# Performance work log

Measured on AMD Instinct MI355X. Metric: run time of the kernel, lower is better.

Reference implementation:

```python
import jax, jax.numpy as jnp
import numpy as np

EMBED_DIM = 1024
NUM_HEADS = 16
HEAD_DIM = EMBED_DIM // NUM_HEADS
MAX_SEQ_LEN = 2048
B, T = 2, 2048


def setup_inputs() -> dict:
    key = jax.random.key(0)
    ks = jax.random.split(key, 12)
    d = EMBED_DIM
    s = lambda fan_in: 1.0 / np.sqrt(fan_in)
    return {
        "x": jax.random.normal(ks[0], (B, T, d), dtype=jnp.float32),
        "ln1_g": jnp.ones((d,), jnp.float32),
        "ln1_b": jnp.zeros((d,), jnp.float32),
        "w_attn": jax.random.normal(ks[1], (d, 3 * d), jnp.float32) * s(d),
        "b_attn": jnp.zeros((3 * d,), jnp.float32),
        "w_proj": jax.random.normal(ks[2], (d, d), jnp.float32) * s(d),
        "b_proj": jnp.zeros((d,), jnp.float32),
        "ln2_g": jnp.ones((d,), jnp.float32),
        "ln2_b": jnp.zeros((d,), jnp.float32),
        "w_fc": jax.random.normal(ks[3], (d, 4 * d), jnp.float32) * s(d),
        "b_fc": jnp.zeros((4 * d,), jnp.float32),
        "w_fc2": jax.random.normal(ks[4], (4 * d, d), jnp.float32) * s(4 * d),
        "b_fc2": jnp.zeros((d,), jnp.float32),
    }


def _layernorm(x, g, b, eps=1e-5):
    mu = jnp.mean(x, axis=-1, keepdims=True)
    var = jnp.var(x, axis=-1, keepdims=True)
    return (x - mu) * jax.lax.rsqrt(var + eps) * g + b


def _attention(x, w_attn, b_attn, w_proj, b_proj):
    b, t, c = x.shape
    qkv = x @ w_attn + b_attn  # [B,T,3C]
    q, k, v = jnp.split(qkv, 3, axis=-1)
    # [B,T,C] -> [B,H,T,Dh]
    rs = lambda a: a.reshape(b, t, NUM_HEADS, HEAD_DIM).transpose(0, 2, 1, 3)
    q, k, v = rs(q), rs(k), rs(v)
    wei = jnp.einsum("bhqd,bhkd->bhqk", q, k) * (HEAD_DIM ** -0.5)
    causal = jnp.tril(jnp.ones((t, t), bool))
    wei = jnp.where(causal, wei, -jnp.inf)
    wei = jax.nn.softmax(wei, axis=-1)  # attn_dropout is identity in eval mode
    out = jnp.einsum("bhqk,bhkd->bhqd", wei, v)
    out = out.transpose(0, 2, 1, 3).reshape(b, t, c)
    return out @ w_proj + b_proj  # resid_dropout identity in eval mode


def _ffn(x, w_fc, b_fc, w_fc2, b_fc2):
    h = jax.nn.gelu(x @ w_fc + b_fc, approximate=False)
    return h @ w_fc2 + b_fc2  # dropout identity in eval mode


def reference(x, ln1_g, ln1_b, w_attn, b_attn, w_proj, b_proj,
              ln2_g, ln2_b, w_fc, b_fc, w_fc2, b_fc2):
    x = x + _attention(_layernorm(x, ln1_g, ln1_b), w_attn, b_attn, w_proj, b_proj)
    x = x + _ffn(_layernorm(x, ln2_g, ln2_b), w_fc, b_fc, w_fc2, b_fc2)
    return x
```

## Files before the change

kernel.cpp:

```cpp
#include <hip/hip_runtime.h>

#define EMBED 1024
#define THREE_EMBED 3072
#define HEADS 16
#define HDIM 64
#define SEQ 2048
#define BATCH 2
#define MTOT 4096

typedef short bf16x8 __attribute__((ext_vector_type(8)));
typedef float f32x4 __attribute__((ext_vector_type(4)));

#define MFMA16(a, b, c) __builtin_amdgcn_mfma_f32_16x16x32_bf16(a, b, c, 0, 0, 0)

__device__ __forceinline__ unsigned short f2bf(float f) {
  union { float f; unsigned int u; } v; v.f = f;
  unsigned int r = v.u + 0x7fffu + ((v.u >> 16) & 1u);
  return (unsigned short)(r >> 16);
}

__device__ __forceinline__ float bf2f(unsigned short u) {
  union { unsigned int u; float f; } v;
  v.u = (unsigned int)u << 16;
  return v.f;
}

__device__ __forceinline__ void gload_lds16(const unsigned short* g, unsigned short* l) {
  __builtin_amdgcn_global_load_lds(
      (const __attribute__((address_space(1))) void*)g,
      (__attribute__((address_space(3))) void*)l, 16, 0, 0);
}

__device__ __forceinline__ void wait_vm0_barrier() {
  asm volatile("s_waitcnt vmcnt(0)" ::: "memory");
  __builtin_amdgcn_s_barrier();
}

template <int N>
__device__ __forceinline__ void wait_vmcnt() {
  if constexpr (N == 0) asm volatile("s_waitcnt vmcnt(0)" ::: "memory");
  else if constexpr (N == 1) asm volatile("s_waitcnt vmcnt(1)" ::: "memory");
  else if constexpr (N == 2) asm volatile("s_waitcnt vmcnt(2)" ::: "memory");
  else if constexpr (N == 3) asm volatile("s_waitcnt vmcnt(3)" ::: "memory");
  else if constexpr (N == 4) asm volatile("s_waitcnt vmcnt(4)" ::: "memory");
  else if constexpr (N == 6) asm volatile("s_waitcnt vmcnt(6)" ::: "memory");
  else if constexpr (N == 8) asm volatile("s_waitcnt vmcnt(8)" ::: "memory");
}

__device__ __forceinline__ void lds_fence() {
  asm volatile("s_waitcnt lgkmcnt(0)" ::: "memory");
  __builtin_amdgcn_sched_barrier(0);
}

__global__ __launch_bounds__(256) void k_transpose_all(
    const float* __restrict__ w_attn, const float* __restrict__ w_proj,
    const float* __restrict__ w_fc, const float* __restrict__ w_fc2,
    unsigned short* __restrict__ o_attn, unsigned short* __restrict__ o_proj,
    unsigned short* __restrict__ o_fc, unsigned short* __restrict__ o_fc2) {
  __shared__ float t[32][33];
  int bid = blockIdx.x;
  const float* in;
  unsigned short* out;
  int K, N, lid;
  if (bid < 3072) {
    in = w_attn; out = o_attn; K = 1024; N = 3072; lid = bid;
  } else if (bid < 4096) {
    in = w_proj; out = o_proj; K = 1024; N = 1024; lid = bid - 3072;
  } else if (bid < 8192) {
    in = w_fc; out = o_fc; K = 1024; N = 4096; lid = bid - 4096;
  } else {
    in = w_fc2; out = o_fc2; K = 4096; N = 1024; lid = bid - 8192;
  }
  int gx = N >> 5;
  int n0 = (lid % gx) * 32, k0 = (lid / gx) * 32;
  int tx = threadIdx.x & 31, ty = threadIdx.x >> 5;
#pragma unroll
  for (int i = 0; i < 32; i += 8)
    t[ty + i][tx] = in[(size_t)(k0 + ty + i) * N + n0 + tx];
  __syncthreads();
#pragma unroll
  for (int i = 0; i < 32; i += 8)
    out[(size_t)(n0 + ty + i) * K + k0 + tx] = f2bf(t[tx][ty + i]);
}

__global__ __launch_bounds__(256) void k_transpose_v(
    const unsigned short* __restrict__ qkv, unsigned short* __restrict__ Vt) {
  __shared__ unsigned short t[32][33];
  int tx = threadIdx.x & 31, ty = threadIdx.x >> 5;
  int t0 = blockIdx.x * 32;
  int d0 = (blockIdx.y & 1) * 32;
  int bh = blockIdx.y >> 1;
  int b = bh >> 4, h = bh & 15;
  const unsigned short* src = qkv + (size_t)b * SEQ * THREE_EMBED + 2 * EMBED + h * HDIM;
#pragma unroll
  for (int i = 0; i < 32; i += 8)
    t[ty + i][tx] = src[(size_t)(t0 + ty + i) * THREE_EMBED + d0 + tx];
  __syncthreads();
  unsigned short* dst = Vt + (size_t)bh * HDIM * SEQ;
#pragma unroll
  for (int i = 0; i < 32; i += 8)
    dst[(size_t)(d0 + ty + i) * SEQ + t0 + tx] = t[tx][ty + i];
}

__global__ __launch_bounds__(256) void k_layernorm(
    const float* __restrict__ x, const float* __restrict__ g,
    const float* __restrict__ b, unsigned short* __restrict__ out) {
  int row = blockIdx.x;
  int tid = threadIdx.x;
  const float4 xv = *(const float4*)(x + (size_t)row * EMBED + tid * 4);
  float s = xv.x + xv.y + xv.z + xv.w;
  float sq = xv.x * xv.x + xv.y * xv.y + xv.z * xv.z + xv.w * xv.w;
#pragma unroll
  for (int off = 1; off < 64; off <<= 1) {
    s += __shfl_xor(s, off);
    sq += __shfl_xor(sq, off);
  }
  __shared__ float red[8];
  int w = tid >> 6;
  if ((tid & 63) == 0) { red[w] = s; red[4 + w] = sq; }
  __syncthreads();
  s = red[0] + red[1] + red[2] + red[3];
  sq = red[4] + red[5] + red[6] + red[7];
  float mu = s * (1.0f / EMBED);
  float var = sq * (1.0f / EMBED) - mu * mu;
  float rs = rsqrtf(var + 1e-5f);
  float xs[4] = {xv.x, xv.y, xv.z, xv.w};
  unsigned short o[4];
#pragma unroll
  for (int c = 0; c < 4; c++) {
    int col = tid * 4 + c;
    o[c] = f2bf((xs[c] - mu) * rs * g[col] + b[col]);
  }
  *(ushort4*)(out + (size_t)row * EMBED + tid * 4) = *(const ushort4*)o;
}

template <int EPI>
__global__ __launch_bounds__(512, 2) void k_gemm8(
    const unsigned short* __restrict__ A, const unsigned short* __restrict__ Bt,
    const float* __restrict__ bias, const float* __restrict__ resid,
    float* __restrict__ outf, unsigned short* __restrict__ outb,
    int M, int N, int K) {
  __shared__ unsigned short lA[2][16384];
  __shared__ unsigned short lB[2][16384];
  int tid = threadIdx.x;
  int nwg = gridDim.x * gridDim.y;
  int bid = blockIdx.y * gridDim.x + blockIdx.x;
  int swz = (bid & 7) * (nwg >> 3) + (bid >> 3);
  int m0 = (swz / gridDim.x) * 256, n0 = (swz % gridDim.x) * 256;
  int lane = tid & 63, w = tid >> 6;
  int lr = lane & 15, lg = lane >> 4;
  int warow = (w >> 2) * 64;
  int wbrow = (w & 3) * 32;
  int rx = lr & 7;
  int colk[2] = {(lg ^ rx) * 8, ((4 + lg) ^ rx) * 8};
  f32x4 acc[8][4] = {};
  int swzk = ((lane & 7) ^ ((lane >> 3) & 7)) * 8;
  const unsigned short* gA[2];
  const unsigned short* gB[2];
#pragma unroll
  for (int i = 0; i < 2; i++) {
    int chrow = (w * 2 + i) * 8 + (lane >> 3);
    gA[i] = A + (size_t)(m0 + chrow) * K + swzk;
    gB[i] = Bt + (size_t)(n0 + chrow) * K + swzk;
  }
  int NT = K >> 6;
  auto stageA = [&](int h, int kt, int buf) {
    size_t goff = (size_t)(h * 128) * K + (size_t)kt * 64;
    int lo = h * 8192 + w * 1024;
    gload_lds16(gA[0] + goff, &lA[buf][lo]);
    gload_lds16(gA[1] + goff, &lA[buf][lo + 512]);
  };
  auto stageB = [&](int h, int kt, int buf) {
    size_t goff = (size_t)(h * 128) * K + (size_t)kt * 64;
    int lo = h * 8192 + w * 1024;
    gload_lds16(gB[0] + goff, &lB[buf][lo]);
    gload_lds16(gB[1] + goff, &lB[buf][lo + 512]);
  };
  bf16x8 aX[4][2], aY[4][2], b0[2][2], b1[2][2];
  auto rdA = [&](int buf, int mh, bf16x8 (&dst)[4][2]) {
#pragma unroll
    for (int ii = 0; ii < 4; ii++) {
      int ra = mh * 128 + warow + ii * 16 + lr;
#pragma unroll
      for (int ks = 0; ks < 2; ks++)
        dst[ii][ks] = *(const bf16x8*)&lA[buf][ra * 64 + colk[ks]];
    }
  };
  auto rdB = [&](int buf, int nh, bf16x8 (&dst)[2][2]) {
#pragma unroll
    for (int jj = 0; jj < 2; jj++) {
      int rb = nh * 128 + wbrow + jj * 16 + lr;
#pragma unroll
      for (int ks = 0; ks < 2; ks++)
        dst[jj][ks] = *(const bf16x8*)&lB[buf][rb * 64 + colk[ks]];
    }
  };
  auto mf = [&](int mh, int nh, bf16x8 (&aa)[4][2], bf16x8 (&bb)[2][2]) {
    __builtin_amdgcn_s_setprio(1);
#pragma unroll
    for (int ii = 0; ii < 4; ii++)
#pragma unroll
      for (int jj = 0; jj < 2; jj++)
#pragma unroll
        for (int ks = 0; ks < 2; ks++)
          acc[mh * 4 + ii][nh * 2 + jj] =
              MFMA16(aa[ii][ks], bb[jj][ks], acc[mh * 4 + ii][nh * 2 + jj]);
    __builtin_amdgcn_s_setprio(0);
  };
  stageA(0, 0, 0); stageB(0, 0, 0);
  stageB(1, 0, 0); stageA(1, 0, 0);
  wait_vmcnt<4>();
  __builtin_amdgcn_s_barrier();
  rdA(0, 0, aX);
  for (int t = 0; t < NT - 1; t++) {
    int cur = t & 1, nxt = cur ^ 1;
    rdB(cur, 0, b0);
    stageA(0, t + 1, nxt); stageB(0, t + 1, nxt);
    wait_vmcnt<4>();
    __builtin_amdgcn_s_barrier();
    lds_fence();
    mf(0, 0, aX, b0);
    rdB(cur, 1, b1);
    rdA(cur, 1, aY);
    __builtin_amdgcn_s_barrier();
    lds_fence();
    mf(0, 1, aX, b1);
    stageB(1, t + 1, nxt); stageA(1, t + 1, nxt);
    wait_vmcnt<4>();
    __builtin_amdgcn_s_barrier();
    lds_fence();
    mf(1, 1, aY, b1);
    rdA(nxt, 0, aX);
    __builtin_amdgcn_s_barrier();
    lds_fence();
    mf(1, 0, aY, b0);
  }
  {
    int cur = (NT - 1) & 1;
    rdB(cur, 0, b0);
    wait_vmcnt<0>();
    __builtin_amdgcn_s_barrier();
    lds_fence();
    mf(0, 0, aX, b0);
    rdB(cur, 1, b1);
    rdA(cur, 1, aY);
    lds_fence();
    mf(0, 1, aX, b1);
    mf(1, 1, aY, b1);
    mf(1, 0, aY, b0);
  }
#pragma unroll
  for (int i = 0; i < 8; i++) {
#pragma unroll
    for (int j = 0; j < 4; j++) {
      int col = n0 + (j >> 1) * 128 + wbrow + (j & 1) * 16 + lr;
      float bv = bias[col];
#pragma unroll
      for (int r = 0; r < 4; r++) {
        int row = m0 + (i >> 2) * 128 + warow + (i & 3) * 16 + lg * 4 + r;
        float v = acc[i][j][r] + bv;
        size_t idx = (size_t)row * N + col;
        if constexpr (EPI == 0) {
          outb[idx] = f2bf(v);
        } else if constexpr (EPI == 1) {
          outf[idx] = v + resid[idx];
        } else {
          float gv = 0.5f * v * (1.0f + erff(v * 0.70710678118654752f));
          outb[idx] = f2bf(gv);
        }
      }
    }
  }
}

template <int EPI>
__global__ __launch_bounds__(256) void k_gemmN(
    const unsigned short* __restrict__ A, const unsigned short* __restrict__ Bt,
    const float* __restrict__ bias, const float* __restrict__ resid,
    float* __restrict__ outf, unsigned short* __restrict__ outb,
    int M, int N, int K) {
  __shared__ unsigned short lA[3][128 * 64];
  __shared__ unsigned short lB[3][64 * 64];
  int tid = threadIdx.x;
  int nwg = gridDim.x * gridDim.y;
  int bid = blockIdx.y * gridDim.x + blockIdx.x;
  int swz = (bid & 7) * (nwg >> 3) + (bid >> 3);
  int m0 = (swz / gridDim.x) * 128, n0 = (swz % gridDim.x) * 64;
  int lane = tid & 63, w = tid >> 6;
  int wm = w * 32;
  int lr = lane & 15, lg = lane >> 4;
  int rx = lr & 7;
  int colk[2] = {(lg ^ rx) * 8, ((4 + lg) ^ rx) * 8};
  f32x4 acc[2][4] = {};
  int swzk = ((lane & 7) ^ ((lane >> 3) & 7)) * 8;
  const unsigned short* gsrc[6];
  int loff[6];
  bool isa[6];
#pragma unroll
  for (int c0 = 0; c0 < 6; c0++) {
    int c = w * 6 + c0;
    if (c < 16) {
      int row = c * 8 + (lane >> 3);
      gsrc[c0] = A + (size_t)(m0 + row) * K + swzk;
      loff[c0] = c * 512;
      isa[c0] = true;
    } else {
      int row = (c - 16) * 8 + (lane >> 3);
      gsrc[c0] = Bt + (size_t)(n0 + row) * K + swzk;
      loff[c0] = (c - 16) * 512;
      isa[c0] = false;
    }
  }
  auto stage = [&](int k0, int buf) {
#pragma unroll
    for (int c0 = 0; c0 < 6; c0++)
      gload_lds16(gsrc[c0] + k0, isa[c0] ? &lA[buf][loff[c0]] : &lB[buf][loff[c0]]);
  };
  auto compute = [&](int buf) {
    bf16x8 af[2][2], bf[4][2];
#pragma unroll
    for (int i = 0; i < 2; i++)
#pragma unroll
      for (int ks = 0; ks < 2; ks++)
        af[i][ks] = *(const bf16x8*)&lA[buf][(wm + i * 16 + lr) * 64 + colk[ks]];
#pragma unroll
    for (int j = 0; j < 4; j++)
#pragma unroll
      for (int ks = 0; ks < 2; ks++)
        bf[j][ks] = *(const bf16x8*)&lB[buf][(j * 16 + lr) * 64 + colk[ks]];
    __builtin_amdgcn_s_setprio(1);
#pragma unroll
    for (int i = 0; i < 2; i++)
#pragma unroll
      for (int j = 0; j < 4; j++)
#pragma unroll
        for (int ks = 0; ks < 2; ks++)
          acc[i][j] = MFMA16(af[i][ks], bf[j][ks], acc[i][j]);
    __builtin_amdgcn_s_setprio(0);
  };
  int nt = K >> 6;
  stage(0, 0);
  stage(64, 1);
  wait_vmcnt<6>();
  __builtin_amdgcn_s_barrier();
  int c0 = 0, c1 = 1, c2 = 2;
  for (int t = 0; t < nt - 2; t++) {
    stage((t + 2) * 64, c2);
    compute(c0);
    wait_vmcnt<6>();
    __builtin_amdgcn_s_barrier();
    int tmp = c0; c0 = c1; c1 = c2; c2 = tmp;
  }
  compute(c0);
  wait_vmcnt<0>();
  __builtin_amdgcn_s_barrier();
  compute(c1);
#pragma unroll
  for (int i = 0; i < 2; i++) {
#pragma unroll
    for (int j = 0; j < 4; j++) {
      int colb = n0 + j * 16 + lr;
      float bv = bias[colb];
#pragma unroll
      for (int r = 0; r < 4; r++) {
        int row = m0 + wm + i * 16 + lg * 4 + r;
        float v = acc[i][j][r] + bv;
        size_t idx = (size_t)row * N + colb;
        if constexpr (EPI == 0) {
          outb[idx] = f2bf(v);
        } else if constexpr (EPI == 1) {
          outf[idx] = v + resid[idx];
        } else {
          float gv = 0.5f * v * (1.0f + erff(v * 0.70710678118654752f));
          outb[idx] = f2bf(gv);
        }
      }
    }
  }
}

__global__ __launch_bounds__(256) void k_attention(
    const unsigned short* __restrict__ qkv, const unsigned short* __restrict__ Vt,
    unsigned short* __restrict__ out) {
  __shared__ unsigned short lK[2][64 * 64];
  __shared__ unsigned short lV[2][64 * 64];
  __shared__ unsigned short lP[4][16][72];
  int bid = blockIdx.x;
  int i = bid >> 3;
  int qt = 31 - (i >> 2);
  int bh = (bid & 7) * 4 + (i & 3);
  int b = bh >> 4, h = bh & 15;
  int tid = threadIdx.x, lane = tid & 63, w = tid >> 6;
  int lr = lane & 15, lg = lane >> 4;
  const unsigned short* base = qkv + (size_t)b * SEQ * THREE_EMBED + h * HDIM;
  const unsigned short* Kb = base + EMBED;
  const unsigned short* Vb = Vt + (size_t)bh * HDIM * SEQ;
  int q0 = qt * 64 + w * 16;
  const float SCL = 0.125f * 1.4426950408889634f;
  bf16x8 qf[2];
  {
    int qrow = q0 + lr;
    bf16x8 r0 = *(const bf16x8*)(base + (size_t)qrow * THREE_EMBED + lg * 8);
    bf16x8 r1 = *(const bf16x8*)(base + (size_t)qrow * THREE_EMBED + 32 + lg * 8);
#pragma unroll
    for (int j = 0; j < 8; j++) {
      qf[0][j] = (short)f2bf(bf2f((unsigned short)r0[j]) * SCL);
      qf[1][j] = (short)f2bf(bf2f((unsigned short)r1[j]) * SCL);
    }
  }
  bf16x8 ones;
  {
    short o1 = 0x3F80;
#pragma unroll
    for (int j = 0; j < 8; j++) ones[j] = o1;
  }
  f32x4 o[4] = {};
  f32x4 osum = {};
  float m_[4] = {-INFINITY, -INFINITY, -INFINITY, -INFINITY};
  int srow = lane >> 3;
  int scol = ((lane & 7) ^ (lane >> 3)) * 8;
  int nkv = qt + 1;
  auto stage = [&](int kt, int cur) {
#pragma unroll
    for (int c = 0; c < 2; c++) {
      int chunk = w * 2 + c;
      int row = chunk * 8 + srow;
      gload_lds16(Kb + (size_t)(kt * 64 + row) * THREE_EMBED + scol, &lK[cur][chunk * 512]);
      gload_lds16(Vb + (size_t)row * SEQ + kt * 64 + scol, &lV[cur][chunk * 512]);
    }
  };
  stage(0, 0);
  wait_vm0_barrier();
  int cur = 0;
  for (int kt = 0; kt < nkv; kt++) {
    if (kt + 1 < nkv) stage(kt + 1, cur ^ 1);
    __builtin_amdgcn_s_setprio(1);
    f32x4 s[4];
#pragma unroll
    for (int ct = 0; ct < 4; ct++) {
      int krow = ct * 16 + lr;
      int sw = (krow & 7) << 3;
      bf16x8 k0 = *(const bf16x8*)&lK[cur][krow * 64 + ((lg * 8) ^ sw)];
      bf16x8 k1 = *(const bf16x8*)&lK[cur][krow * 64 + ((32 + lg * 8) ^ sw)];
      f32x4 z = {};
      z = MFMA16(qf[0], k0, z);
      s[ct] = MFMA16(qf[1], k1, z);
    }
    __builtin_amdgcn_s_setprio(0);
    bool maskt = (kt * 64 + 63 > q0);
    float pm[4] = {-INFINITY, -INFINITY, -INFINITY, -INFINITY};
#pragma unroll
    for (int ct = 0; ct < 4; ct++) {
#pragma unroll
      for (int r = 0; r < 4; r++) {
        float sv = s[ct][r];
        if (maskt) {
          int kg = kt * 64 + ct * 16 + lr;
          int qg = q0 + lg * 4 + r;
          if (kg > qg) sv = -INFINITY;
        }
        s[ct][r] = sv;
        pm[r] = fmaxf(pm[r], sv);
      }
    }
    float dm = fmaxf(fmaxf(pm[0] - m_[0], pm[1] - m_[1]),
                     fmaxf(pm[2] - m_[2], pm[3] - m_[3]));
    if (!__all(dm <= 8.0f)) {
#pragma unroll
      for (int r = 0; r < 4; r++) {
        float mx = pm[r];
        mx = fmaxf(mx, __shfl_xor(mx, 1));
        mx = fmaxf(mx, __shfl_xor(mx, 2));
        mx = fmaxf(mx, __shfl_xor(mx, 4));
        mx = fmaxf(mx, __shfl_xor(mx, 8));
        float mn = fmaxf(m_[r], mx);
        float al = exp2f(m_[r] - mn);
        m_[r] = mn;
        osum[r] *= al;
#pragma unroll
        for (int dt = 0; dt < 4; dt++) o[dt][r] *= al;
      }
    }
#pragma unroll
    for (int ct = 0; ct < 4; ct++) {
#pragma unroll
      for (int rp = 0; rp < 2; rp++) {
        float p0 = exp2f(s[ct][2 * rp] - m_[2 * rp]);
        float p1 = exp2f(s[ct][2 * rp + 1] - m_[2 * rp + 1]);
        unsigned int pk;
        asm("v_cvt_pk_bf16_f32 %0, %1, %2" : "=v"(pk) : "v"(p0), "v"(p1));
        lP[w][lg * 4 + 2 * rp][ct * 16 + lr] = (unsigned short)pk;
        lP[w][lg * 4 + 2 * rp + 1][ct * 16 + lr] = (unsigned short)(pk >> 16);
      }
    }
    __builtin_amdgcn_s_setprio(1);
#pragma unroll
    for (int ks = 0; ks < 2; ks++) {
      bf16x8 pf = *(const bf16x8*)&lP[w][lr][ks * 32 + lg * 8];
      osum = MFMA16(pf, ones, osum);
#pragma unroll
      for (int dt = 0; dt < 4; dt++) {
        int vrow = dt * 16 + lr;
        int sw = (vrow & 7) << 3;
        bf16x8 vf = *(const bf16x8*)&lV[cur][vrow * 64 + ((ks * 32 + lg * 8) ^ sw)];
        o[dt] = MFMA16(pf, vf, o[dt]);
      }
    }
    __builtin_amdgcn_s_setprio(0);
    wait_vm0_barrier();
    cur ^= 1;
  }
#pragma unroll
  for (int dt = 0; dt < 4; dt++)
#pragma unroll
    for (int r = 0; r < 4; r++) {
      int row = q0 + lg * 4 + r;
      float val = o[dt][r] / osum[r];
      out[(size_t)(b * SEQ + row) * EMBED + h * HDIM + dt * 16 + lr] = f2bf(val);
    }
}

extern "C" void kernel_launch(void* const* d_in, const int* in_sizes, int n_in,
                              void* d_out, int out_size, void* d_ws, size_t ws_size,
                              hipStream_t stream) {
  const float* x      = (const float*)d_in[0];
  const float* ln1_g  = (const float*)d_in[1];
  const float* ln1_b  = (const float*)d_in[2];
  const float* w_attn = (const float*)d_in[3];
  const float* b_attn = (const float*)d_in[4];
  const float* w_proj = (const float*)d_in[5];
  const float* b_proj = (const float*)d_in[6];
  const float* ln2_g  = (const float*)d_in[7];
  const float* ln2_b  = (const float*)d_in[8];
  const float* w_fc   = (const float*)d_in[9];
  const float* b_fc   = (const float*)d_in[10];
  const float* w_fc2  = (const float*)d_in[11];
  const float* b_fc2  = (const float*)d_in[12];
  float* outp = (float*)d_out;

  char* ws = (char*)d_ws;
  unsigned short* wT_attn = (unsigned short*)(ws);
  unsigned short* wT_proj = (unsigned short*)(ws + 6291456);
  unsigned short* wT_fc   = (unsigned short*)(ws + 8388608);
  unsigned short* wT_fc2  = (unsigned short*)(ws + 16777216);
  unsigned short* buf1    = (unsigned short*)(ws + 25165824);
  float*          x1      = (float*)(ws + 33554432);
  unsigned short* Vt      = (unsigned short*)(ws + 33554432);
  unsigned short* qkv_h   = (unsigned short*)(ws + 50331648);

  dim3 blk(256);
  k_transpose_all<<<dim3(12288), blk, 0, stream>>>(
      w_attn, w_proj, w_fc, w_fc2, wT_attn, wT_proj, wT_fc, wT_fc2);
  k_layernorm<<<dim3(MTOT), blk, 0, stream>>>(x, ln1_g, ln1_b, buf1);
  k_gemm8<0><<<dim3(THREE_EMBED / 256, MTOT / 256), dim3(512), 0, stream>>>(
      buf1, wT_attn, b_attn, nullptr, nullptr, qkv_h, MTOT, THREE_EMBED, EMBED);
  k_transpose_v<<<dim3(SEQ / 32, 2 * BATCH * HEADS), blk, 0, stream>>>(qkv_h, Vt);
  k_attention<<<dim3(1024), blk, 0, stream>>>(qkv_h, Vt, buf1);
  k_gemmN<1><<<dim3(EMBED / 64, MTOT / 128), blk, 0, stream>>>(
      buf1, wT_proj, b_proj, x, x1, nullptr, MTOT, EMBED, EMBED);
  k_layernorm<<<dim3(MTOT), blk, 0, stream>>>(x1, ln2_g, ln2_b, buf1);
  k_gemm8<2><<<dim3(4 * EMBED / 256, MTOT / 256), dim3(512), 0, stream>>>(
      buf1, wT_fc, b_fc, nullptr, nullptr, qkv_h, MTOT, 4 * EMBED, EMBED);
  k_gemmN<1><<<dim3(EMBED / 64, MTOT / 128), blk, 0, stream>>>(
      qkv_h, wT_fc2, b_fc2, x1, outp, nullptr, MTOT, EMBED, 4 * EMBED);
}
```

Baseline: 233.0 us.

## Split attention KV loop across wave pairs with 32-row query tiles

Each attention block now handles 32 query rows instead of 64, so the grid doubles to 2048 blocks. Two waves share each 16-row query slice and process alternating KV tiles, staging two KV tiles per iteration. Their partial softmax states are merged through LDS at the end. This is meant to raise parallelism and shorten the per-block critical path on the causal attention. In exchange it adds the LDS merge step, doubles LDS use for K/V, and reads Q from global twice as many times.

```diff
diff --git a/kernel.cpp b/kernel.cpp
--- a/kernel.cpp
+++ b/kernel.cpp
@@ -382,20 +382,21 @@
 __global__ __launch_bounds__(256) void k_attention(
     const unsigned short* __restrict__ qkv, const unsigned short* __restrict__ Vt,
     unsigned short* __restrict__ out) {
-  __shared__ unsigned short lK[2][64 * 64];
-  __shared__ unsigned short lV[2][64 * 64];
+  __shared__ unsigned short lK[2][2][4096];
+  __shared__ unsigned short lV[2][2][4096];
   __shared__ unsigned short lP[4][16][72];
   int bid = blockIdx.x;
   int i = bid >> 3;
-  int qt = 31 - (i >> 2);
+  int qt = 63 - (i >> 2);
   int bh = (bid & 7) * 4 + (i & 3);
   int b = bh >> 4, h = bh & 15;
   int tid = threadIdx.x, lane = tid & 63, w = tid >> 6;
+  int qh = w >> 1, p = w & 1;
   int lr = lane & 15, lg = lane >> 4;
   const unsigned short* base = qkv + (size_t)b * SEQ * THREE_EMBED + h * HDIM;
   const unsigned short* Kb = base + EMBED;
   const unsigned short* Vb = Vt + (size_t)bh * HDIM * SEQ;
-  int q0 = qt * 64 + w * 16;
+  int q0 = qt * 32 + qh * 16;
   const float SCL = 0.125f * 1.4426950408889634f;
   bf16x8 qf[2];
   {
@@ -419,105 +420,141 @@
   float m_[4] = {-INFINITY, -INFINITY, -INFINITY, -INFINITY};
   int srow = lane >> 3;
   int scol = ((lane & 7) ^ (lane >> 3)) * 8;
-  int nkv = qt + 1;
-  auto stage = [&](int kt, int cur) {
-#pragma unroll
-    for (int c = 0; c < 2; c++) {
-      int chunk = w * 2 + c;
-      int row = chunk * 8 + srow;
-      gload_lds16(Kb + (size_t)(kt * 64 + row) * THREE_EMBED + scol, &lK[cur][chunk * 512]);
-      gload_lds16(Vb + (size_t)row * SEQ + kt * 64 + scol, &lV[cur][chunk * 512]);
-    }
-  };
-  stage(0, 0);
+  int nkv = (qt >> 1) + 1;
+  int npairs = (nkv + 1) >> 1;
+  auto stagePair = [&](int j, int buf) {
+#pragma unroll
+    for (int c0 = 0; c0 < 8; c0++) {
+      int c = w * 8 + c0;
+      int ts = c >> 4;
+      int kt = 2 * j + ts;
+      if (kt >= nkv) continue;
+      int isV = (c >> 3) & 1;
+      int sub = c & 7;
+      int row = sub * 8 + srow;
+      if (!isV)
+        gload_lds16(Kb + (size_t)(kt * 64 + row) * THREE_EMBED + scol, &lK[buf][ts][sub * 512]);
+      else
+        gload_lds16(Vb + (size_t)row * SEQ + kt * 64 + scol, &lV[buf][ts][sub * 512]);
+    }
+  };
+  stagePair(0, 0);
   wait_vm0_barrier();
-  int cur = 0;
-  for (int kt = 0; kt < nkv; kt++) {
-    if (kt + 1 < nkv) stage(kt + 1, cur ^ 1);
-    __builtin_amdgcn_s_setprio(1);
-    f32x4 s[4];
-#pragma unroll
-    for (int ct = 0; ct < 4; ct++) {
-      int krow = ct * 16 + lr;
-      int sw = (krow & 7) << 3;
-      bf16x8 k0 = *(const bf16x8*)&lK[cur][krow * 64 + ((lg * 8) ^ sw)];
-      bf16x8 k1 = *(const bf16x8*)&lK[cur][krow * 64 + ((32 + lg * 8) ^ sw)];
-      f32x4 z = {};
-      z = MFMA16(qf[0], k0, z);
-      s[ct] = MFMA16(qf[1], k1, z);
-    }
-    __builtin_amdgcn_s_setprio(0);
-    bool maskt = (kt * 64 + 63 > q0);
-    float pm[4] = {-INFINITY, -INFINITY, -INFINITY, -INFINITY};
-#pragma unroll
-    for (int ct = 0; ct < 4; ct++) {
+  int buf = 0;
+  for (int j = 0; j < npairs; j++) {
+    if (j + 1 < npairs) stagePair(j + 1, buf ^ 1);
+    int kt = 2 * j + p;
+    if (kt < nkv) {
+      __builtin_amdgcn_s_setprio(1);
+      f32x4 s[4];
+#pragma unroll
+      for (int ct = 0; ct < 4; ct++) {
+        int krow = ct * 16 + lr;
+        int sw = (krow & 7) << 3;
+        bf16x8 k0 = *(const bf16x8*)&lK[buf][p][krow * 64 + ((lg * 8) ^ sw)];
+        bf16x8 k1 = *(const bf16x8*)&lK[buf][p][krow * 64 + ((32 + lg * 8) ^ sw)];
+        f32x4 z = {};
+        z = MFMA16(qf[0], k0, z);
+        s[ct] = MFMA16(qf[1], k1, z);
+      }
+      __builtin_amdgcn_s_setprio(0);
+      bool maskt = (kt * 64 + 63 > q0);
+      float pm[4] = {-INFINITY, -INFINITY, -INFINITY, -INFINITY};
+#pragma unroll
+      for (int ct = 0; ct < 4; ct++) {
+#pragma unroll
+        for (int r = 0; r < 4; r++) {
+          float sv = s[ct][r];
+          if (maskt) {
+            int kg = kt * 64 + ct * 16 + lr;
+            int qg = q0 + lg * 4 + r;
+            if (kg > qg) sv = -INFINITY;
+          }
+          s[ct][r] = sv;
+          pm[r] = fmaxf(pm[r], sv);
+        }
+      }
+      float dm = fmaxf(fmaxf(pm[0] - m_[0], pm[1] - m_[1]),
+                       fmaxf(pm[2] - m_[2], pm[3] - m_[3]));
+      if (!__all(dm <= 8.0f)) {
+#pragma unroll
+        for (int r = 0; r < 4; r++) {
+          float mx = pm[r];
+          mx = fmaxf(mx, __shfl_xor(mx, 1));
+          mx = fmaxf(mx, __shfl_xor(mx, 2));
+          mx = fmaxf(mx, __shfl_xor(mx, 4));
+          mx = fmaxf(mx, __shfl_xor(mx, 8));
+          float mn = fmaxf(m_[r], mx);
+          float al = exp2f(m_[r] - mn);
+          m_[r] = mn;
+          osum[r] *= al;
+#pragma unroll
+          for (int dt = 0; dt < 4; dt++) o[dt][r] *= al;
+        }
+      }
+#pragma unroll
+      for (int ct = 0; ct < 4; ct++) {
+#pragma unroll
+        for (int rp = 0; rp < 2; rp++) {
+          float p0 = exp2f(s[ct][2 * rp] - m_[2 * rp]);
+          float p1 = exp2f(s[ct][2 * rp + 1] - m_[2 * rp + 1]);
+          unsigned int pk;
+          asm("v_cvt_pk_bf16_f32 %0, %1, %2" : "=v"(pk) : "v"(p0), "v"(p1));
+          lP[w][lg * 4 + 2 * rp][ct * 16 + lr] = (unsigned short)pk;
+          lP[w][lg * 4 + 2 * rp + 1][ct * 16 + lr] = (unsigned short)(pk >> 16);
+        }
+      }
+      __builtin_amdgcn_s_setprio(1);
+#pragma unroll
+      for (int ks = 0; ks < 2; ks++) {
+        bf16x8 pf = *(const bf16x8*)&lP[w][lr][ks * 32 + lg * 8];
+        osum = MFMA16(pf, ones, osum);
+#pragma unroll
+        for (int dt = 0; dt < 4; dt++) {
+          int vrow = dt * 16 + lr;
+          int sw = (vrow & 7) << 3;
+          bf16x8 vf = *(const bf16x8*)&lV[buf][p][vrow * 64 + ((ks * 32 + lg * 8) ^ sw)];
+          o[dt] = MFMA16(pf, vf, o[dt]);
+        }
+      }
+      __builtin_amdgcn_s_setprio(0);
+    }
+    wait_vm0_barrier();
+    buf ^= 1;
+  }
+  float* pb = (float*)&lK[0][0][0] + qh * 1600;
+  if (p == 1) {
+    float* dst = pb + lane * 25;
+#pragma unroll
+    for (int dt = 0; dt < 4; dt++)
+#pragma unroll
+      for (int r = 0; r < 4; r++) dst[dt * 4 + r] = o[dt][r];
+#pragma unroll
+    for (int r = 0; r < 4; r++) { dst[16 + r] = osum[r]; dst[20 + r] = m_[r]; }
+  }
+  __syncthreads();
+  if (p == 0) {
+    const float* src = pb + lane * 25;
+#pragma unroll
+    for (int r = 0; r < 4; r++) {
+      float m1 = src[20 + r];
+      float M = fmaxf(m_[r], m1);
+      float s0 = exp2f(m_[r] - M);
+      float s1 = exp2f(m1 - M);
+      osum[r] = osum[r] * s0 + src[16 + r] * s1;
+#pragma unroll
+      for (int dt = 0; dt < 4; dt++)
+        o[dt][r] = o[dt][r] * s0 + src[dt * 4 + r] * s1;
+    }
+#pragma unroll
+    for (int dt = 0; dt < 4; dt++)
 #pragma unroll
       for (int r = 0; r < 4; r++) {
-        float sv = s[ct][r];
-        if (maskt) {
-          int kg = kt * 64 + ct * 16 + lr;
-          int qg = q0 + lg * 4 + r;
-          if (kg > qg) sv = -INFINITY;
-        }
-        s[ct][r] = sv;
-        pm[r] = fmaxf(pm[r], sv);
-      }
-    }
-    float dm = fmaxf(fmaxf(pm[0] - m_[0], pm[1] - m_[1]),
-                     fmaxf(pm[2] - m_[2], pm[3] - m_[3]));
-    if (!__all(dm <= 8.0f)) {
-#pragma unroll
-      for (int r = 0; r < 4; r++) {
-        float mx = pm[r];
-        mx = fmaxf(mx, __shfl_xor(mx, 1));
-        mx = fmaxf(mx, __shfl_xor(mx, 2));
-        mx = fmaxf(mx, __shfl_xor(mx, 4));
-        mx = fmaxf(mx, __shfl_xor(mx, 8));
-        float mn = fmaxf(m_[r], mx);
-        float al = exp2f(m_[r] - mn);
-        m_[r] = mn;
-        osum[r] *= al;
-#pragma unroll
-        for (int dt = 0; dt < 4; dt++) o[dt][r] *= al;
-      }
-    }
-#pragma unroll
-    for (int ct = 0; ct < 4; ct++) {
-#pragma unroll
-      for (int rp = 0; rp < 2; rp++) {
-        float p0 = exp2f(s[ct][2 * rp] - m_[2 * rp]);
-        float p1 = exp2f(s[ct][2 * rp + 1] - m_[2 * rp + 1]);
-        unsigned int pk;
-        asm("v_cvt_pk_bf16_f32 %0, %1, %2" : "=v"(pk) : "v"(p0), "v"(p1));
-        lP[w][lg * 4 + 2 * rp][ct * 16 + lr] = (unsigned short)pk;
-        lP[w][lg * 4 + 2 * rp + 1][ct * 16 + lr] = (unsigned short)(pk >> 16);
-      }
-    }
-    __builtin_amdgcn_s_setprio(1);
-#pragma unroll
-    for (int ks = 0; ks < 2; ks++) {
-      bf16x8 pf = *(const bf16x8*)&lP[w][lr][ks * 32 + lg * 8];
-      osum = MFMA16(pf, ones, osum);
-#pragma unroll
-      for (int dt = 0; dt < 4; dt++) {
-        int vrow = dt * 16 + lr;
-        int sw = (vrow & 7) << 3;
-        bf16x8 vf = *(const bf16x8*)&lV[cur][vrow * 64 + ((ks * 32 + lg * 8) ^ sw)];
-        o[dt] = MFMA16(pf, vf, o[dt]);
-      }
-    }
-    __builtin_amdgcn_s_setprio(0);
-    wait_vm0_barrier();
-    cur ^= 1;
-  }
-#pragma unroll
-  for (int dt = 0; dt < 4; dt++)
-#pragma unroll
-    for (int r = 0; r < 4; r++) {
-      int row = q0 + lg * 4 + r;
-      float val = o[dt][r] / osum[r];
-      out[(size_t)(b * SEQ + row) * EMBED + h * HDIM + dt * 16 + lr] = f2bf(val);
-    }
+        int row = q0 + lg * 4 + r;
+        float val = o[dt][r] / osum[r];
+        out[(size_t)(b * SEQ + row) * EMBED + h * HDIM + dt * 16 + lr] = f2bf(val);
+      }
+  }
 }
 
 extern "C" void kernel_launch(void* const* d_in, const int* in_sizes, int n_in,
@@ -555,7 +592,7 @@
   k_gemm8<0><<<dim3(THREE_EMBED / 256, MTOT / 256), dim3(512), 0, stream>>>(
       buf1, wT_attn, b_attn, nullptr, nullptr, qkv_h, MTOT, THREE_EMBED, EMBED);
   k_transpose_v<<<dim3(SEQ / 32, 2 * BATCH * HEADS), blk, 0, stream>>>(qkv_h, Vt);
-  k_attention<<<dim3(1024), blk, 0, stream>>>(qkv_h, Vt, buf1);
+  k_attention<<<dim3(2048), blk, 0, stream>>>(qkv_h, Vt, buf1);
   k_gemmN<1><<<dim3(EMBED / 64, MTOT / 128), blk, 0, stream>>>(
       buf1, wT_proj, b_proj, x, x1, nullptr, MTOT, EMBED, EMBED);
   k_layernorm<<<dim3(MTOT), blk, 0, stream>>>(x1, ln2_g, ln2_b, buf1);
```

After: 250.5 us, median of 2. +7.5%, slower.
